# Kernel tuning notes

Measured on AMD Instinct MI355X. Metric: run time of the kernel, lower is better.

Reference implementation:

```python
import jax, jax.numpy as jnp
import numpy as np

B, S, HID, H = 2, 2048, 1024, 16
D = HID // H
LAMBDA_INIT = 0.8
GN_EPS = 1e-5


def setup_inputs() -> dict:
    rng = jax.random.key(0)
    ks = jax.random.split(rng, 12)
    w = 0.02
    return {
        "query": jax.random.normal(ks[0], (B, S, HID), dtype=jnp.float32),
        "key": jax.random.normal(ks[1], (B, S, HID), dtype=jnp.float32),
        "value": jax.random.normal(ks[2], (B, S, HID), dtype=jnp.float32),
        "attention_mask": jnp.ones((B, S), dtype=jnp.float32),
        # params ([in, out] layout; x @ W)
        "Wq": jax.random.normal(ks[3], (HID, H * D * 2), dtype=jnp.float32) * w,
        "Wk": jax.random.normal(ks[4], (HID, H * D * 2), dtype=jnp.float32) * w,
        "Wv": jax.random.normal(ks[5], (HID, H * D), dtype=jnp.float32) * w,
        "Wo": jax.random.normal(ks[6], (H * D, HID), dtype=jnp.float32) * w,
        "lam_q1": jax.random.normal(ks[7], (D,), dtype=jnp.float32),
        "lam_q2": jax.random.normal(ks[8], (D,), dtype=jnp.float32),
        "lam_k1": jax.random.normal(ks[9], (D,), dtype=jnp.float32),
        "lam_k2": jax.random.normal(ks[10], (D,), dtype=jnp.float32),
        "gn_weight": jnp.ones((H * D,), dtype=jnp.float32),
        "gn_bias": jnp.zeros((H * D,), dtype=jnp.float32),
    }


def reference(query, key, value, attention_mask, Wq, Wk, Wv, Wo,
              lam_q1, lam_q2, lam_k1, lam_k2, gn_weight, gn_bias):
    b, s, hid = query.shape
    h, d = H, hid // H
    rs = 1.0 / jnp.sqrt(jnp.asarray(d, query.dtype))

    q = (query @ Wq).reshape(b, s, h, 2 * d).transpose(0, 2, 1, 3)   # [b,h,s,2d]
    k = (key @ Wk).reshape(b, s, h, 2 * d).transpose(0, 2, 1, 3)
    v = (value @ Wv).reshape(b, s, h, d).transpose(0, 2, 1, 3)       # [b,h,s,d]

    Q1, Q2 = q[..., :d], q[..., d:]
    K1, K2 = k[..., :d], k[..., d:]
    s1 = jnp.einsum('bhqd,bhkd->bhqk', Q1, K1) * rs
    s2 = jnp.einsum('bhqd,bhkd->bhqk', Q2, K2) * rs

    # ALiBi bias: slopes[h] * (pos_q - pos_k), subtracted from scores
    pos = jnp.arange(s, dtype=query.dtype)
    slopes = 2.0 ** (-8.0 * jnp.arange(1, h + 1, dtype=query.dtype) / h)
    alibi = slopes[None, :, None, None] * (pos[:, None] - pos[None, :])[None, None]
    causal = jnp.triu(jnp.full((s, s), -1e9, dtype=query.dtype), k=1)[None, None]
    pad = (1.0 - attention_mask)[:, None, None, :] * -1e9
    add = -alibi + causal + pad

    w1 = jax.nn.softmax(s1 + add, axis=-1)
    w2 = jax.nn.softmax(s2 + add, axis=-1)

    lam = (jnp.exp(jnp.dot(lam_q1, lam_k1))
           - jnp.exp(jnp.dot(lam_q2, lam_k2)) + LAMBDA_INIT)
    dw = w1 - lam * w2

    attn = jnp.einsum('bhqk,bhkd->bhqd', dw, v).transpose(0, 2, 1, 3)  # [b,s,h,d]

    # GroupNorm(groups=h, channels=h*d) over [b, C, L]: per (b, head) normalize over (seq, d)
    mean = attn.mean(axis=(1, 3), keepdims=True)
    var = ((attn - mean) ** 2).mean(axis=(1, 3), keepdims=True)
    normed = (attn - mean) / jnp.sqrt(var + GN_EPS)
    normed = normed * gn_weight.reshape(1, 1, h, d) + gn_bias.reshape(1, 1, h, d)

    out = normed * (1.0 - LAMBDA_INIT)
    return out.reshape(b, s, h * d) @ Wo
```

## Files before the change

kernel.cpp:

```cpp
#include <hip/hip_runtime.h>
#include <cstdint>
#include <cstddef>

#define SQ 2048
#define NH 16
#define DH 64
#define HIDN 1024

typedef __attribute__((ext_vector_type(8))) short bf16x8;
typedef __attribute__((ext_vector_type(4))) float f32x4;
typedef __attribute__((ext_vector_type(2))) unsigned u32x2;

__device__ inline short f2b(float x) {
  union { float f; unsigned u; } un; un.f = x;
  unsigned r = un.u + 0x7fffu + ((un.u >> 16) & 1u);
  return (short)(r >> 16);
}

__device__ inline unsigned cvt_pk(float lo, float hi) {
  unsigned r;
  asm("v_cvt_pk_bf16_f32 %0, %1, %2" : "=v"(r) : "v"(lo), "v"(hi));
  return r;
}

__device__ inline f32x4 mfma16(u32x2 a, u32x2 b, f32x4 c) {
  asm("v_mfma_f32_16x16x16_bf16 %0, %1, %2, %0" : "+v"(c) : "v"(a), "v"(b));
  return c;
}

__device__ inline void gl_lds16(const void* g, void* l) {
  __builtin_amdgcn_global_load_lds(
      (const __attribute__((address_space(1))) void*)g,
      (__attribute__((address_space(3))) void*)l, 16, 0, 0);
}

__global__ __launch_bounds__(256) void qkv_to_bf16(const float4* __restrict__ q,
                                                   const float4* __restrict__ k,
                                                   const float4* __restrict__ v,
                                                   short4* __restrict__ out) {
  int i = blockIdx.x * 256 + threadIdx.x;
  const float4* src = (i < 1048576) ? q : ((i < 2097152) ? k : v);
  float4 val = src[i & 1048575];
  short4 o;
  o.x = f2b(val.x); o.y = f2b(val.y); o.z = f2b(val.z); o.w = f2b(val.w);
  out[i] = o;
}

__global__ __launch_bounds__(256) void wconv4(const float* __restrict__ Wq,
                                              const float* __restrict__ Wk,
                                              const float* __restrict__ Wv,
                                              const float* __restrict__ Wo,
                                              short* __restrict__ WqT, short* __restrict__ WkT,
                                              short* __restrict__ WvT, short* __restrict__ WoT) {
  __shared__ float t[32][33];
  int z = blockIdx.z;
  int N = (z < 2) ? 2048 : 1024;
  if (blockIdx.x * 32 >= N) return;
  const float* W = (z == 0) ? Wq : (z == 1) ? Wk : (z == 2) ? Wv : Wo;
  short* Wt = (z == 0) ? WqT : (z == 1) ? WkT : (z == 2) ? WvT : WoT;
  const int K = 1024;
  int n0 = blockIdx.x * 32, k0 = blockIdx.y * 32;
  int tx = threadIdx.x & 31, ty = threadIdx.x >> 5;
#pragma unroll
  for (int r = 0; r < 4; ++r)
    t[ty + r * 8][tx] = W[(size_t)(k0 + ty + r * 8) * N + n0 + tx];
  __syncthreads();
#pragma unroll
  for (int r = 0; r < 4; ++r)
    Wt[(size_t)(n0 + ty + r * 8) * K + k0 + tx] = f2b(t[tx][ty + r * 8]);
}

__global__ void lam_k(const float* __restrict__ q1, const float* __restrict__ q2,
                      const float* __restrict__ k1, const float* __restrict__ k2,
                      float* __restrict__ out) {
  int i = threadIdx.x;
  float d1 = q1[i] * k1[i], d2 = q2[i] * k2[i];
#pragma unroll
  for (int x = 1; x < 64; x <<= 1) { d1 += __shfl_xor(d1, x); d2 += __shfl_xor(d2, x); }
  if (i == 0) out[0] = __expf(d1) - __expf(d2) + 0.8f;
}

__global__ __launch_bounds__(256) void padk(const float* __restrict__ mask,
                                            float* __restrict__ padl2) {
  int i = blockIdx.x * 256 + threadIdx.x;
  padl2[i] = (1.0f - mask[i]) * (-1.0e9f) * 1.44269504089f;
}

__global__ __launch_bounds__(256) void proj3(const short* __restrict__ Abase,
                                             const short* __restrict__ Btbase,
                                             short* __restrict__ QKout,
                                             short* __restrict__ Vtb) {
  const int z = blockIdx.z;
  if (z == 2 && blockIdx.x >= 8) return;
  const int K = 1024;
  const short* A = Abase + (size_t)z * 4194304;
  const short* Bt = Btbase + (size_t)z * 2097152;

  __shared__ __align__(16) short As[128 * 64];
  __shared__ __align__(16) short Bs[128 * 64];
  const int tid = threadIdx.x;
  const int lane = tid & 63, w = tid >> 6;
  const int l15 = lane & 15, lhi = lane >> 4;
  const int wr = w >> 1, wc = w & 1;
  const int m0 = blockIdx.y * 128, n0 = blockIdx.x * 128;

  f32x4 acc[4][4];
#pragma unroll
  for (int i = 0; i < 4; ++i)
#pragma unroll
    for (int j = 0; j < 4; ++j) acc[i][j] = (f32x4){0.f, 0.f, 0.f, 0.f};

  const short* Ag = A + (size_t)m0 * K;
  const short* Bg = Bt + (size_t)n0 * K;

  for (int k0 = 0; k0 < K; k0 += 64) {
#pragma unroll
    for (int it = 0; it < 4; ++it) {
      int idx = it * 256 + tid;
      int row = idx >> 3, c8 = (idx & 7) << 3;
      gl_lds16(Ag + (size_t)row * K + (k0 + c8), &As[idx << 3]);
      gl_lds16(Bg + (size_t)row * K + (k0 + c8), &Bs[idx << 3]);
    }
    __syncthreads();
#pragma unroll
    for (int kk = 0; kk < 64; kk += 32) {
      bf16x8 af[4], bfr[4];
#pragma unroll
      for (int mi = 0; mi < 4; ++mi)
        af[mi] = *(const bf16x8*)&As[(wr * 64 + mi * 16 + l15) * 64 + kk + lhi * 8];
#pragma unroll
      for (int ni = 0; ni < 4; ++ni)
        bfr[ni] = *(const bf16x8*)&Bs[(wc * 64 + ni * 16 + l15) * 64 + kk + lhi * 8];
#pragma unroll
      for (int mi = 0; mi < 4; ++mi)
#pragma unroll
        for (int ni = 0; ni < 4; ++ni)
          acc[mi][ni] = __builtin_amdgcn_mfma_f32_16x16x32_bf16(af[mi], bfr[ni], acc[mi][ni], 0, 0, 0);
    }
    __syncthreads();
  }

#pragma unroll
  for (int mi = 0; mi < 4; ++mi) {
#pragma unroll
    for (int ni = 0; ni < 4; ++ni) {
#pragma unroll
      for (int j = 0; j < 4; ++j) {
        int m = m0 + wr * 64 + mi * 16 + (lhi << 2) + j;
        int n = n0 + wc * 64 + ni * 16 + l15;
        float v = acc[mi][ni][j];
        int s = m & (SQ - 1), bb = m >> 11;
        if (z < 2) {
          int h = n >> 7, t = n & 127, path = t >> 6, tt = t & 63;
          (QKout + (size_t)z * 8388608)
              [((((size_t)(bb * NH + h) * 2 + path) * SQ + s) << 6) + tt] = f2b(v);
        } else {
          int h = n >> 6, t = n & 63;
          Vtb[(((size_t)(bb * NH + h) << 6) + t) * SQ + s] = f2b(v);
        }
      }
    }
  }
}

__global__ __launch_bounds__(256) void gemm_out(const short* __restrict__ A,
                                                const short* __restrict__ Bt,
                                                float* __restrict__ Cout) {
  const int N = 1024, K = 1024;
  __shared__ __align__(16) short As[128 * 64];
  __shared__ __align__(16) short Bs[128 * 64];
  const int tid = threadIdx.x;
  const int lane = tid & 63, w = tid >> 6;
  const int l15 = lane & 15, lhi = lane >> 4;
  const int wr = w >> 1, wc = w & 1;
  const int m0 = blockIdx.y * 128, n0 = blockIdx.x * 128;

  f32x4 acc[4][4];
#pragma unroll
  for (int i = 0; i < 4; ++i)
#pragma unroll
    for (int j = 0; j < 4; ++j) acc[i][j] = (f32x4){0.f, 0.f, 0.f, 0.f};

  const short* Ag = A + (size_t)m0 * K;
  const short* Bg = Bt + (size_t)n0 * K;

  for (int k0 = 0; k0 < K; k0 += 64) {
#pragma unroll
    for (int it = 0; it < 4; ++it) {
      int idx = it * 256 + tid;
      int row = idx >> 3, c8 = (idx & 7) << 3;
      gl_lds16(Ag + (size_t)row * K + (k0 + c8), &As[idx << 3]);
      gl_lds16(Bg + (size_t)row * K + (k0 + c8), &Bs[idx << 3]);
    }
    __syncthreads();
#pragma unroll
    for (int kk = 0; kk < 64; kk += 32) {
      bf16x8 af[4], bfr[4];
#pragma unroll
      for (int mi = 0; mi < 4; ++mi)
        af[mi] = *(const bf16x8*)&As[(wr * 64 + mi * 16 + l15) * 64 + kk + lhi * 8];
#pragma unroll
      for (int ni = 0; ni < 4; ++ni)
        bfr[ni] = *(const bf16x8*)&Bs[(wc * 64 + ni * 16 + l15) * 64 + kk + lhi * 8];
#pragma unroll
      for (int mi = 0; mi < 4; ++mi)
#pragma unroll
        for (int ni = 0; ni < 4; ++ni)
          acc[mi][ni] = __builtin_amdgcn_mfma_f32_16x16x32_bf16(af[mi], bfr[ni], acc[mi][ni], 0, 0, 0);
    }
    __syncthreads();
  }

#pragma unroll
  for (int mi = 0; mi < 4; ++mi)
#pragma unroll
    for (int ni = 0; ni < 4; ++ni)
#pragma unroll
      for (int j = 0; j < 4; ++j) {
        int m = m0 + wr * 64 + mi * 16 + (lhi << 2) + j;
        int n = n0 + wc * 64 + ni * 16 + l15;
        Cout[(size_t)m * N + n] = acc[mi][ni][j];
      }
}

__global__ __launch_bounds__(128) void diff_attn(
    const short* __restrict__ Qp, const short* __restrict__ Kp,
    const short* __restrict__ Vt, const float* __restrict__ padl2,
    const float* __restrict__ lamp, float* __restrict__ attn,
    float* __restrict__ part) {
  __shared__ __align__(16) short K1s[64 * 64];
  __shared__ __align__(16) short K2s[64 * 64];
  __shared__ __align__(16) short Vts[64 * 64];
  __shared__ float red[4];

  const int bid = blockIdx.x;
  const int rk = bid >> 5, bh = bid & 31;
  const int st = 63 - rk;
  const int b = bh >> 4, h = bh & 15;
  const int tid = threadIdx.x, lane = tid & 63, w = tid >> 6;
  const int l15 = lane & 15, lhi = lane >> 4;
  const int sw7 = l15 & 7;
  const int u0 = (lhi ^ sw7) << 3, u1 = ((4 + lhi) ^ sw7) << 3;
  const int ktmax = st >> 1;
  const int wq0 = st * 32 + (w << 4);
  const int q = wq0 + l15;

  const float slope = exp2f(-0.5f * (float)(h + 1));
  const float L2E = 1.44269504089f;
  const float SC = 0.125f * L2E;
  const float sl2 = slope * L2E;
  const float s64 = sl2 * 64.0f;
  const float qb8 = sl2 * (float)q + 8.0f;

  f32x4 c4m[4];
#pragma unroll
  for (int cf = 0; cf < 4; ++cf)
#pragma unroll
    for (int j = 0; j < 4; ++j)
      c4m[cf][j] = sl2 * (float)(16 * cf + 4 * lhi + j) - qb8;

  const short* Q1g = Qp + (((size_t)bh * 2 + 0) * SQ) * DH;
  const short* Q2g = Qp + (((size_t)bh * 2 + 1) * SQ) * DH;
  const short* K1g = Kp + (((size_t)bh * 2 + 0) * SQ) * DH;
  const short* K2g = Kp + (((size_t)bh * 2 + 1) * SQ) * DH;
  const short* Vtg = Vt + (size_t)bh * DH * SQ;
  const float* padb = padl2 + (b << 11);

  bf16x8 aq[2][2];
#pragma unroll
  for (int kk = 0; kk < 2; ++kk) {
    aq[0][kk] = *(const bf16x8*)&Q1g[(size_t)q * DH + kk * 32 + lhi * 8];
    aq[1][kk] = *(const bf16x8*)&Q2g[(size_t)q * DH + kk * 32 + lhi * 8];
  }

  int ucf[4];
#pragma unroll
  for (int cf = 0; cf < 4; ++cf)
    ucf[cf] = (((2 * cf + (lhi >> 1)) ^ sw7) << 1) + (lhi & 1);

  f32x4 acc[2][4];
  float ll[2] = {0.f, 0.f};
#pragma unroll
  for (int p = 0; p < 2; ++p)
#pragma unroll
    for (int i = 0; i < 4; ++i) acc[p][i] = (f32x4){0.f, 0.f, 0.f, 0.f};

  for (int kt = 0; kt <= ktmax; ++kt) {
    const int k0 = kt * 64;
#pragma unroll
    for (int it = 0; it < 4; ++it) {
      int idx = it * 128 + tid;
      int row = idx >> 3, u = idx & 7;
      int us = (u ^ (row & 7)) << 3;
      gl_lds16(K1g + (size_t)(k0 + row) * DH + us, &K1s[idx << 3]);
      gl_lds16(K2g + (size_t)(k0 + row) * DH + us, &K2s[idx << 3]);
      gl_lds16(Vtg + (size_t)row * SQ + k0 + us, &Vts[idx << 3]);
    }
    __syncthreads();

    f32x4 base4[4];
#pragma unroll
    for (int cf = 0; cf < 4; ++cf) {
      f32x4 p4 = *(const f32x4*)&padb[k0 + 16 * cf + 4 * lhi];
#pragma unroll
      for (int j = 0; j < 4; ++j) base4[cf][j] = c4m[cf][j] + p4[j];
    }
#pragma unroll
    for (int cf = 0; cf < 4; ++cf)
#pragma unroll
      for (int j = 0; j < 4; ++j) c4m[cf][j] += s64;
    const bool diag = (kt == ktmax);

    u32x2 pa[2][4];
#pragma unroll
    for (int p = 0; p < 2; ++p) {
      const short* Ks = (p == 0) ? K1s : K2s;
      f32x4 sv[4];
#pragma unroll
      for (int cf = 0; cf < 4; ++cf) {
        int rb = (cf * 16 + l15) << 6;
        f32x4 z = (f32x4){0.f, 0.f, 0.f, 0.f};
        bf16x8 ka = *(const bf16x8*)&Ks[rb + u0];
        bf16x8 kb = *(const bf16x8*)&Ks[rb + u1];
        sv[cf] = __builtin_amdgcn_mfma_f32_16x16x32_bf16(ka, aq[p][0], z, 0, 0, 0);
        sv[cf] = __builtin_amdgcn_mfma_f32_16x16x32_bf16(kb, aq[p][1], sv[cf], 0, 0, 0);
      }
      float rsum = 0.f;
#pragma unroll
      for (int cf = 0; cf < 4; ++cf) {
        float pv[4];
#pragma unroll
        for (int j = 0; j < 4; ++j) pv[j] = sv[cf][j] * SC + base4[cf][j];
        if (diag) {
#pragma unroll
          for (int j = 0; j < 4; ++j) {
            int kc = k0 + 16 * cf + 4 * lhi + j;
            pv[j] = (kc > q) ? -1.0e9f : pv[j];
          }
        }
        float e0 = exp2f(pv[0]);
        float e1 = exp2f(pv[1]);
        float e2 = exp2f(pv[2]);
        float e3 = exp2f(pv[3]);
        rsum += (e0 + e1) + (e2 + e3);
        pa[p][cf][0] = cvt_pk(e0, e1);
        pa[p][cf][1] = cvt_pk(e2, e3);
      }
      ll[p] += rsum;
    }

#pragma unroll
    for (int df = 0; df < 4; ++df) {
      const u32x2* vrow = (const u32x2*)&Vts[(df * 16 + l15) << 6];
#pragma unroll
      for (int cf = 0; cf < 4; ++cf) {
        u32x2 vb = vrow[ucf[cf]];
        acc[0][df] = mfma16(pa[0][cf], vb, acc[0][df]);
        acc[1][df] = mfma16(pa[1][cf], vb, acc[1][df]);
      }
    }
    __syncthreads();
  }

#pragma unroll
  for (int p = 0; p < 2; ++p) {
    ll[p] += __shfl_xor(ll[p], 16);
    ll[p] += __shfl_xor(ll[p], 32);
  }
  float lamv = lamp[0];
  float li1 = 1.0f / ll[0], li2 = lamv / ll[1];
  float li1b[4], li2b[4];
#pragma unroll
  for (int j = 0; j < 4; ++j) {
    li1b[j] = __shfl(li1, (lhi << 2) + j);
    li2b[j] = __shfl(li2, (lhi << 2) + j);
  }
  float lsum = 0.f, lsq = 0.f;
#pragma unroll
  for (int df = 0; df < 4; ++df)
#pragma unroll
    for (int j = 0; j < 4; ++j) {
      int qq = wq0 + (lhi << 2) + j;
      float o = acc[0][df][j] * li1b[j] - acc[1][df][j] * li2b[j];
      attn[((size_t)b * SQ + qq) * HIDN + (h << 6) + (df << 4) + l15] = o;
      lsum += o; lsq += o * o;
    }
#pragma unroll
  for (int x = 1; x < 64; x <<= 1) {
    lsum += __shfl_xor(lsum, x);
    lsq += __shfl_xor(lsq, x);
  }
  if (lane == 0) { red[w] = lsum; red[2 + w] = lsq; }
  __syncthreads();
  if (tid == 0) {
    part[((size_t)bh * 64 + st) * 2] = red[0] + red[1];
    part[((size_t)bh * 64 + st) * 2 + 1] = red[2] + red[3];
  }
}

__global__ void stats_fin(const float* __restrict__ part, float* __restrict__ mi) {
  int bh = threadIdx.x;
  float s = 0.f, ss = 0.f;
  for (int t = 0; t < 64; ++t) {
    s += part[(bh * 64 + t) * 2];
    ss += part[(bh * 64 + t) * 2 + 1];
  }
  float n = (float)(SQ * DH);
  float mean = s / n;
  float var = ss / n - mean * mean;
  mi[bh * 2] = mean;
  mi[bh * 2 + 1] = rsqrtf(var + 1e-5f);
}

__global__ __launch_bounds__(256) void gn_apply(const float* __restrict__ attn,
                                                const float* __restrict__ mi,
                                                const float* __restrict__ gnw,
                                                const float* __restrict__ gnb,
                                                short* __restrict__ X) {
  size_t i = (size_t)blockIdx.x * 256 + threadIdx.x;
  size_t base = i << 2;
  int r = (int)(base >> 10);
  int c = (int)(base & 1023);
  int bh = ((r >> 11) << 4) + (c >> 6);
  float mean = mi[bh * 2], inv = mi[bh * 2 + 1];
  float4 a = *(const float4*)&attn[base];
  short4 o;
  o.x = f2b(((a.x - mean) * inv * gnw[c + 0] + gnb[c + 0]) * 0.2f);
  o.y = f2b(((a.y - mean) * inv * gnw[c + 1] + gnb[c + 1]) * 0.2f);
  o.z = f2b(((a.z - mean) * inv * gnw[c + 2] + gnb[c + 2]) * 0.2f);
  o.w = f2b(((a.w - mean) * inv * gnw[c + 3] + gnb[c + 3]) * 0.2f);
  *(short4*)&X[base] = o;
}

extern "C" void kernel_launch(void* const* d_in, const int* in_sizes, int n_in,
                              void* d_out, int out_size, void* d_ws, size_t ws_size,
                              hipStream_t stream) {
  const float* query = (const float*)d_in[0];
  const float* key = (const float*)d_in[1];
  const float* value = (const float*)d_in[2];
  const float* mask = (const float*)d_in[3];
  const float* Wq = (const float*)d_in[4];
  const float* Wk = (const float*)d_in[5];
  const float* Wv = (const float*)d_in[6];
  const float* Wo = (const float*)d_in[7];
  const float* lq1 = (const float*)d_in[8];
  const float* lq2 = (const float*)d_in[9];
  const float* lk1 = (const float*)d_in[10];
  const float* lk2 = (const float*)d_in[11];
  const float* gnw = (const float*)d_in[12];
  const float* gnb = (const float*)d_in[13];

  char* ws = (char*)d_ws;
  short* WqT = (short*)(ws + 0);
  short* WkT = (short*)(ws + 4194304);
  short* WvT = (short*)(ws + 8388608);
  short* WoT = (short*)(ws + 10485760);
  short* qb = (short*)(ws + 12582912);
  short* Qp = (short*)(ws + 37748736);
  short* Kp = (short*)(ws + 54525952);
  short* Vtb = (short*)(ws + 71303168);
  float* attn = (float*)(ws + 12582912);
  short* X = (short*)(ws + 29360128);
  float* part = (float*)(ws + 79691776);
  float* mi = (float*)(ws + 79708160);
  float* lam = (float*)(ws + 79708416);
  float* padl2 = (float*)(ws + 79708672);

  qkv_to_bf16<<<12288, 256, 0, stream>>>((const float4*)query, (const float4*)key,
                                         (const float4*)value, (short4*)qb);
  wconv4<<<dim3(64, 32, 4), 256, 0, stream>>>(Wq, Wk, Wv, Wo, WqT, WkT, WvT, WoT);
  lam_k<<<1, 64, 0, stream>>>(lq1, lq2, lk1, lk2, lam);
  padk<<<16, 256, 0, stream>>>(mask, padl2);

  proj3<<<dim3(16, 32, 3), 256, 0, stream>>>(qb, WqT, Qp, Vtb);

  diff_attn<<<dim3(2048), 128, 0, stream>>>(Qp, Kp, Vtb, padl2, lam, attn, part);
  stats_fin<<<1, 32, 0, stream>>>(part, mi);
  gn_apply<<<4096, 256, 0, stream>>>(attn, mi, gnw, gnb, X);
  gemm_out<<<dim3(8, 32), 256, 0, stream>>>(X, WoT, (float*)d_out);
}
```

Before: 245.9 us.

## Double-buffer K/V tiles and pair causal query tiles per block

```diff
diff --git a/kernel.cpp b/kernel.cpp
--- a/kernel.cpp
+++ b/kernel.cpp
@@ -223,41 +223,37 @@
       }
 }
 
-__global__ __launch_bounds__(128) void diff_attn(
+__global__ __launch_bounds__(256) void diff_attn(
     const short* __restrict__ Qp, const short* __restrict__ Kp,
     const short* __restrict__ Vt, const float* __restrict__ padl2,
     const float* __restrict__ lamp, float* __restrict__ attn,
     float* __restrict__ part) {
-  __shared__ __align__(16) short K1s[64 * 64];
-  __shared__ __align__(16) short K2s[64 * 64];
-  __shared__ __align__(16) short Vts[64 * 64];
-  __shared__ float red[4];
+  __shared__ __align__(16) short K1s[2][64 * 64];
+  __shared__ __align__(16) short K2s[2][64 * 64];
+  __shared__ __align__(16) short Vts[2][64 * 64];
+  __shared__ float red[8];
 
   const int bid = blockIdx.x;
   const int rk = bid >> 5, bh = bid & 31;
-  const int st = 63 - rk;
+  const int qtA = 31 - rk, qtB = rk;
+  const int ntA = qtA + 1, ntT = ntA + qtB + 1;
   const int b = bh >> 4, h = bh & 15;
   const int tid = threadIdx.x, lane = tid & 63, w = tid >> 6;
   const int l15 = lane & 15, lhi = lane >> 4;
   const int sw7 = l15 & 7;
   const int u0 = (lhi ^ sw7) << 3, u1 = ((4 + lhi) ^ sw7) << 3;
-  const int ktmax = st >> 1;
-  const int wq0 = st * 32 + (w << 4);
-  const int q = wq0 + l15;
-
+
+  const float L2E = 1.44269504089f;
   const float slope = exp2f(-0.5f * (float)(h + 1));
-  const float L2E = 1.44269504089f;
   const float SC = 0.125f * L2E;
   const float sl2 = slope * L2E;
-  const float s64 = sl2 * 64.0f;
-  const float qb8 = sl2 * (float)q + 8.0f;
-
-  f32x4 c4m[4];
+
+  f32x4 ck[4];
 #pragma unroll
   for (int cf = 0; cf < 4; ++cf)
 #pragma unroll
     for (int j = 0; j < 4; ++j)
-      c4m[cf][j] = sl2 * (float)(16 * cf + 4 * lhi + j) - qb8;
+      ck[cf][j] = sl2 * (float)(16 * cf + 4 * lhi + j);
 
   const short* Q1g = Qp + (((size_t)bh * 2 + 0) * SQ) * DH;
   const short* Q2g = Qp + (((size_t)bh * 2 + 1) * SQ) * DH;
@@ -266,144 +262,174 @@
   const short* Vtg = Vt + (size_t)bh * DH * SQ;
   const float* padb = padl2 + (b << 11);
 
-  bf16x8 aq[2][2];
-#pragma unroll
-  for (int kk = 0; kk < 2; ++kk) {
-    aq[0][kk] = *(const bf16x8*)&Q1g[(size_t)q * DH + kk * 32 + lhi * 8];
-    aq[1][kk] = *(const bf16x8*)&Q2g[(size_t)q * DH + kk * 32 + lhi * 8];
-  }
-
   int ucf[4];
 #pragma unroll
   for (int cf = 0; cf < 4; ++cf)
     ucf[cf] = (((2 * cf + (lhi >> 1)) ^ sw7) << 1) + (lhi & 1);
 
-  f32x4 acc[2][4];
-  float ll[2] = {0.f, 0.f};
-#pragma unroll
-  for (int p = 0; p < 2; ++p)
-#pragma unroll
-    for (int i = 0; i < 4; ++i) acc[p][i] = (f32x4){0.f, 0.f, 0.f, 0.f};
-
-  for (int kt = 0; kt <= ktmax; ++kt) {
-    const int k0 = kt * 64;
-#pragma unroll
-    for (int it = 0; it < 4; ++it) {
-      int idx = it * 128 + tid;
-      int row = idx >> 3, u = idx & 7;
-      int us = (u ^ (row & 7)) << 3;
-      gl_lds16(K1g + (size_t)(k0 + row) * DH + us, &K1s[idx << 3]);
-      gl_lds16(K2g + (size_t)(k0 + row) * DH + us, &K2s[idx << 3]);
-      gl_lds16(Vtg + (size_t)row * SQ + k0 + us, &Vts[idx << 3]);
-    }
+  const int sidx0 = tid, sidx1 = 256 + tid;
+  const int srow0 = sidx0 >> 3, sus0 = ((sidx0 & 7) ^ (srow0 & 7)) << 3;
+  const int srow1 = sidx1 >> 3, sus1 = ((sidx1 & 7) ^ (srow1 & 7)) << 3;
+
+#define STAGE(buf, k0s)                                                          \
+  {                                                                              \
+    gl_lds16(K1g + (size_t)((k0s) + srow0) * DH + sus0, &K1s[buf][sidx0 << 3]);  \
+    gl_lds16(K2g + (size_t)((k0s) + srow0) * DH + sus0, &K2s[buf][sidx0 << 3]);  \
+    gl_lds16(Vtg + (size_t)srow0 * SQ + (k0s) + sus0, &Vts[buf][sidx0 << 3]);    \
+    gl_lds16(K1g + (size_t)((k0s) + srow1) * DH + sus1, &K1s[buf][sidx1 << 3]);  \
+    gl_lds16(K2g + (size_t)((k0s) + srow1) * DH + sus1, &K2s[buf][sidx1 << 3]);  \
+    gl_lds16(Vtg + (size_t)srow1 * SQ + (k0s) + sus1, &Vts[buf][sidx1 << 3]);    \
+  }
+
+  int cur = 0;
+  int itg = 0;
+  STAGE(0, 0);
+  asm volatile("s_waitcnt vmcnt(0)" ::: "memory");
+  __builtin_amdgcn_s_barrier();
+
+  const float lamv = lamp[0];
+
+  for (int ph = 0; ph < 2; ++ph) {
+    const int qt = ph ? qtB : qtA;
+    const int nt = qt + 1;
+    const int wq0 = qt * 64 + (w << 4);
+    const int q = wq0 + l15;
+    const float qb8 = sl2 * (float)q + 8.0f;
+
+    bf16x8 aq[2][2];
+#pragma unroll
+    for (int kk = 0; kk < 2; ++kk) {
+      aq[0][kk] = *(const bf16x8*)&Q1g[(size_t)q * DH + kk * 32 + lhi * 8];
+      aq[1][kk] = *(const bf16x8*)&Q2g[(size_t)q * DH + kk * 32 + lhi * 8];
+    }
+    f32x4 cq[4];
+#pragma unroll
+    for (int cf = 0; cf < 4; ++cf)
+#pragma unroll
+      for (int j = 0; j < 4; ++j) cq[cf][j] = ck[cf][j] - qb8;
+
+    f32x4 acc[2][4];
+    float ll[2] = {0.f, 0.f};
+#pragma unroll
+    for (int p = 0; p < 2; ++p)
+#pragma unroll
+      for (int i = 0; i < 4; ++i) acc[p][i] = (f32x4){0.f, 0.f, 0.f, 0.f};
+
+    for (int kt = 0; kt < nt; ++kt, ++itg) {
+      const int k0 = kt << 6;
+      int g = itg + 1;
+      if (g < ntT) {
+        int k0n = ((g < ntA) ? g : g - ntA) << 6;
+        STAGE(cur ^ 1, k0n);
+      }
+
+      const float t0 = sl2 * (float)k0;
+      f32x4 base4[4];
+#pragma unroll
+      for (int cf = 0; cf < 4; ++cf) {
+        f32x4 p4 = *(const f32x4*)&padb[k0 + 16 * cf + 4 * lhi];
+#pragma unroll
+        for (int j = 0; j < 4; ++j) base4[cf][j] = cq[cf][j] + (t0 + p4[j]);
+      }
+      const bool diag = (kt == nt - 1);
+
+      u32x2 pa[2][4];
+#pragma unroll
+      for (int p = 0; p < 2; ++p) {
+        const short* Ks = (p == 0) ? K1s[cur] : K2s[cur];
+        f32x4 sv[4];
+#pragma unroll
+        for (int cf = 0; cf < 4; ++cf) {
+          int rb = (cf * 16 + l15) << 6;
+          f32x4 z = (f32x4){0.f, 0.f, 0.f, 0.f};
+          bf16x8 ka = *(const bf16x8*)&Ks[rb + u0];
+          bf16x8 kb = *(const bf16x8*)&Ks[rb + u1];
+          sv[cf] = __builtin_amdgcn_mfma_f32_16x16x32_bf16(ka, aq[p][0], z, 0, 0, 0);
+          sv[cf] = __builtin_amdgcn_mfma_f32_16x16x32_bf16(kb, aq[p][1], sv[cf], 0, 0, 0);
+        }
+        float rsum = 0.f;
+#pragma unroll
+        for (int cf = 0; cf < 4; ++cf) {
+          float pv[4];
+#pragma unroll
+          for (int j = 0; j < 4; ++j) pv[j] = sv[cf][j] * SC + base4[cf][j];
+          if (diag) {
+#pragma unroll
+            for (int j = 0; j < 4; ++j) {
+              int kc = k0 + 16 * cf + 4 * lhi + j;
+              pv[j] = (kc > q) ? -1.0e9f : pv[j];
+            }
+          }
+          float e0 = exp2f(pv[0]);
+          float e1 = exp2f(pv[1]);
+          float e2 = exp2f(pv[2]);
+          float e3 = exp2f(pv[3]);
+          rsum += (e0 + e1) + (e2 + e3);
+          pa[p][cf][0] = cvt_pk(e0, e1);
+          pa[p][cf][1] = cvt_pk(e2, e3);
+        }
+        ll[p] += rsum;
+      }
+
+#pragma unroll
+      for (int df = 0; df < 4; ++df) {
+        const u32x2* vrow = (const u32x2*)&Vts[cur][(df * 16 + l15) << 6];
+#pragma unroll
+        for (int cf = 0; cf < 4; ++cf) {
+          u32x2 vb = vrow[ucf[cf]];
+          acc[0][df] = mfma16(pa[0][cf], vb, acc[0][df]);
+          acc[1][df] = mfma16(pa[1][cf], vb, acc[1][df]);
+        }
+      }
+
+      asm volatile("s_waitcnt vmcnt(0)" ::: "memory");
+      __builtin_amdgcn_s_barrier();
+      cur ^= 1;
+    }
+
+#pragma unroll
+    for (int p = 0; p < 2; ++p) {
+      ll[p] += __shfl_xor(ll[p], 16);
+      ll[p] += __shfl_xor(ll[p], 32);
+    }
+    float li1 = 1.0f / ll[0], li2 = lamv / ll[1];
+    float li1b[4], li2b[4];
+#pragma unroll
+    for (int j = 0; j < 4; ++j) {
+      li1b[j] = __shfl(li1, (lhi << 2) + j);
+      li2b[j] = __shfl(li2, (lhi << 2) + j);
+    }
+    float lsum = 0.f, lsq = 0.f;
+#pragma unroll
+    for (int df = 0; df < 4; ++df)
+#pragma unroll
+      for (int j = 0; j < 4; ++j) {
+        int qq = wq0 + (lhi << 2) + j;
+        float o = acc[0][df][j] * li1b[j] - acc[1][df][j] * li2b[j];
+        attn[((size_t)b * SQ + qq) * HIDN + (h << 6) + (df << 4) + l15] = o;
+        lsum += o; lsq += o * o;
+      }
+#pragma unroll
+    for (int x = 1; x < 64; x <<= 1) {
+      lsum += __shfl_xor(lsum, x);
+      lsq += __shfl_xor(lsq, x);
+    }
+    if (lane == 0) { red[w] = lsum; red[4 + w] = lsq; }
     __syncthreads();
-
-    f32x4 base4[4];
-#pragma unroll
-    for (int cf = 0; cf < 4; ++cf) {
-      f32x4 p4 = *(const f32x4*)&padb[k0 + 16 * cf + 4 * lhi];
-#pragma unroll
-      for (int j = 0; j < 4; ++j) base4[cf][j] = c4m[cf][j] + p4[j];
-    }
-#pragma unroll
-    for (int cf = 0; cf < 4; ++cf)
-#pragma unroll
-      for (int j = 0; j < 4; ++j) c4m[cf][j] += s64;
-    const bool diag = (kt == ktmax);
-
-    u32x2 pa[2][4];
-#pragma unroll
-    for (int p = 0; p < 2; ++p) {
-      const short* Ks = (p == 0) ? K1s : K2s;
-      f32x4 sv[4];
-#pragma unroll
-      for (int cf = 0; cf < 4; ++cf) {
-        int rb = (cf * 16 + l15) << 6;
-        f32x4 z = (f32x4){0.f, 0.f, 0.f, 0.f};
-        bf16x8 ka = *(const bf16x8*)&Ks[rb + u0];
-        bf16x8 kb = *(const bf16x8*)&Ks[rb + u1];
-        sv[cf] = __builtin_amdgcn_mfma_f32_16x16x32_bf16(ka, aq[p][0], z, 0, 0, 0);
-        sv[cf] = __builtin_amdgcn_mfma_f32_16x16x32_bf16(kb, aq[p][1], sv[cf], 0, 0, 0);
-      }
-      float rsum = 0.f;
-#pragma unroll
-      for (int cf = 0; cf < 4; ++cf) {
-        float pv[4];
-#pragma unroll
-        for (int j = 0; j < 4; ++j) pv[j] = sv[cf][j] * SC + base4[cf][j];
-        if (diag) {
-#pragma unroll
-          for (int j = 0; j < 4; ++j) {
-            int kc = k0 + 16 * cf + 4 * lhi + j;
-            pv[j] = (kc > q) ? -1.0e9f : pv[j];
-          }
-        }
-        float e0 = exp2f(pv[0]);
-        float e1 = exp2f(pv[1]);
-        float e2 = exp2f(pv[2]);
-        float e3 = exp2f(pv[3]);
-        rsum += (e0 + e1) + (e2 + e3);
-        pa[p][cf][0] = cvt_pk(e0, e1);
-        pa[p][cf][1] = cvt_pk(e2, e3);
-      }
-      ll[p] += rsum;
-    }
-
-#pragma unroll
-    for (int df = 0; df < 4; ++df) {
-      const u32x2* vrow = (const u32x2*)&Vts[(df * 16 + l15) << 6];
-#pragma unroll
-      for (int cf = 0; cf < 4; ++cf) {
-        u32x2 vb = vrow[ucf[cf]];
-        acc[0][df] = mfma16(pa[0][cf], vb, acc[0][df]);
-        acc[1][df] = mfma16(pa[1][cf], vb, acc[1][df]);
-      }
-    }
-    __syncthreads();
+    if (tid == 0) {
+      part[((size_t)bh * 32 + qt) * 2] = red[0] + red[1] + red[2] + red[3];
+      part[((size_t)bh * 32 + qt) * 2 + 1] = red[4] + red[5] + red[6] + red[7];
+    }
   }
-
-#pragma unroll
-  for (int p = 0; p < 2; ++p) {
-    ll[p] += __shfl_xor(ll[p], 16);
-    ll[p] += __shfl_xor(ll[p], 32);
-  }
-  float lamv = lamp[0];
-  float li1 = 1.0f / ll[0], li2 = lamv / ll[1];
-  float li1b[4], li2b[4];
-#pragma unroll
-  for (int j = 0; j < 4; ++j) {
-    li1b[j] = __shfl(li1, (lhi << 2) + j);
-    li2b[j] = __shfl(li2, (lhi << 2) + j);
-  }
-  float lsum = 0.f, lsq = 0.f;
-#pragma unroll
-  for (int df = 0; df < 4; ++df)
-#pragma unroll
-    for (int j = 0; j < 4; ++j) {
-      int qq = wq0 + (lhi << 2) + j;
-      float o = acc[0][df][j] * li1b[j] - acc[1][df][j] * li2b[j];
-      attn[((size_t)b * SQ + qq) * HIDN + (h << 6) + (df << 4) + l15] = o;
-      lsum += o; lsq += o * o;
-    }
-#pragma unroll
-  for (int x = 1; x < 64; x <<= 1) {
-    lsum += __shfl_xor(lsum, x);
-    lsq += __shfl_xor(lsq, x);
-  }
-  if (lane == 0) { red[w] = lsum; red[2 + w] = lsq; }
-  __syncthreads();
-  if (tid == 0) {
-    part[((size_t)bh * 64 + st) * 2] = red[0] + red[1];
-    part[((size_t)bh * 64 + st) * 2 + 1] = red[2] + red[3];
-  }
+#undef STAGE
 }
 
 __global__ void stats_fin(const float* __restrict__ part, float* __restrict__ mi) {
   int bh = threadIdx.x;
   float s = 0.f, ss = 0.f;
-  for (int t = 0; t < 64; ++t) {
-    s += part[(bh * 64 + t) * 2];
-    ss += part[(bh * 64 + t) * 2 + 1];
+  for (int t = 0; t < 32; ++t) {
+    s += part[(bh * 32 + t) * 2];
+    ss += part[(bh * 32 + t) * 2 + 1];
   }
   float n = (float)(SQ * DH);
   float mean = s / n;
@@ -474,7 +500,7 @@
 
   proj3<<<dim3(16, 32, 3), 256, 0, stream>>>(qb, WqT, Qp, Vtb);
 
-  diff_attn<<<dim3(2048), 128, 0, stream>>>(Qp, Kp, Vtb, padl2, lam, attn, part);
+  diff_attn<<<dim3(512), 256, 0, stream>>>(Qp, Kp, Vtb, padl2, lam, attn, part);
   stats_fin<<<1, 32, 0, stream>>>(part, mi);
   gn_apply<<<4096, 256, 0, stream>>>(attn, mi, gnw, gnb, X);
   gemm_out<<<dim3(8, 32), 256, 0, stream>>>(X, WoT, (float*)d_out);
```

Result: faster. 226.3 us (-8.0%).
